# Kernel tuning notes

Hardware: AMD Instinct MI355X
Metric: run time of the kernel (lower is better)

## Reference

```python
import jax, jax.numpy as jnp
import numpy as np

N_HEADS = 16
K_CH = 1024 // N_HEADS  # 64
SCALE = 1.0 / np.sqrt(K_CH)


def setup_inputs() -> dict:
    key = jax.random.key(0)
    ks = jax.random.split(key, 10)
    B, C, T = 4, 1024, 2048
    Cout = 1024
    xavier = lambda k, o, i: jax.random.uniform(k, (o, i), jnp.float32, -1.0, 1.0) * np.sqrt(6.0 / (o + i))
    return {
        "x": jax.random.normal(ks[0], (B, C, T), jnp.float32),
        "c": jax.random.normal(ks[1], (B, C, T), jnp.float32),
        "Wq": xavier(ks[2], C, C), "bq": jnp.zeros((C,), jnp.float32),
        "Wk": xavier(ks[3], C, C), "bk": jnp.zeros((C,), jnp.float32),
        "Wv": xavier(ks[4], C, C), "bv": jnp.zeros((C,), jnp.float32),
        "Wo": xavier(ks[5], Cout, C), "bo": jnp.zeros((Cout,), jnp.float32),
    }


def reference(x, c, Wq, bq, Wk, bk, Wv, bv, Wo, bo):
    B, C, T = x.shape
    H, K = N_HEADS, K_CH
    # 1x1 Conv1d == per-timestep linear: [O,C] @ [B,C,T] -> [B,O,T]
    q = jnp.einsum('oc,bct->bot', Wq, x) + bq[None, :, None]
    k = jnp.einsum('oc,bct->bot', Wk, c) + bk[None, :, None]
    v = jnp.einsum('oc,bct->bot', Wv, c) + bv[None, :, None]
    # split heads: b (h k) t -> b h k t
    q = q.reshape(B, H, K, T)
    k = k.reshape(B, H, K, -1)
    v = v.reshape(B, H, K, -1)
    scores = jnp.einsum('bhkt,bhks->bhts', q, k) * SCALE  # [B,H,Tt,Ts]
    p = jax.nn.softmax(scores, axis=-1)
    out = jnp.einsum('bhts,bhks->bhkt', p, v)  # b h k t
    out = out.reshape(B, H * K, T)
    return jnp.einsum('oc,bct->bot', Wo, out) + bo[None, :, None]
```

## Files before the change

kernel.cpp:

```cpp
#include <hip/hip_runtime.h>
#include <stdint.h>

typedef __bf16 bf16x8 __attribute__((ext_vector_type(8)));
typedef float f32x4 __attribute__((ext_vector_type(4)));
typedef float f32x16 __attribute__((ext_vector_type(16)));
typedef unsigned u32x2 __attribute__((ext_vector_type(2)));
typedef unsigned u32x4 __attribute__((ext_vector_type(4)));

#define LOG2E 1.44269504088896340736f
#define ATT_SCALE 0.125f
#define CL (ATT_SCALE * LOG2E)
#define SWZ(row, colb) ((colb) ^ (((row) & 7) << 4))

#define GLOAD_LDS16(gp, lp)                                                  \
  __builtin_amdgcn_global_load_lds(                                          \
      (const __attribute__((address_space(1))) void*)(gp),                   \
      (__attribute__((address_space(3))) void*)(lp), 16, 0, 0)

__device__ __forceinline__ unsigned short f2bf(float f) {
  unsigned int x = __float_as_uint(f);
  x += 0x7fffu + ((x >> 16) & 1u);
  return (unsigned short)(x >> 16);
}

__device__ __forceinline__ float fexp2(float x) {
#if __has_builtin(__builtin_amdgcn_exp2f)
  return __builtin_amdgcn_exp2f(x);
#else
  return exp2f(x);
#endif
}

__device__ __forceinline__ unsigned cvtpk(float lo, float hi) {
  unsigned r;
  asm("v_cvt_pk_bf16_f32 %0, %1, %2" : "=v"(r) : "v"(lo), "v"(hi));
  return r;
}

__device__ __forceinline__ u32x2 plswap(unsigned a, unsigned b) {
  asm("v_permlane32_swap_b32 %0, %1" : "+v"(a), "+v"(b));
  u32x2 r;
  r[0] = a;
  r[1] = b;
  return r;
}

__global__ __launch_bounds__(256) void prep_inputs(
    const float* __restrict__ x, const float* __restrict__ c,
    const float* __restrict__ Wq, const float* __restrict__ Wk,
    const float* __restrict__ Wv, const float* __restrict__ Wo,
    unsigned short* __restrict__ xT, unsigned short* __restrict__ cT,
    unsigned short* __restrict__ wqb, unsigned short* __restrict__ wkb,
    unsigned short* __restrict__ wvb, unsigned short* __restrict__ wob) {
  const int C = 1024, T = 2048;
  int z = blockIdx.z;
  if (z >= 8) {
    int sel = z - 8;
    int bi = blockIdx.y * 64 + blockIdx.x;
    if (bi >= 512) return;
    const float* in = sel == 0 ? Wq : sel == 1 ? Wk : sel == 2 ? Wv : Wo;
    unsigned short* out = sel == 0 ? wqb : sel == 1 ? wkb : sel == 2 ? wvb : wob;
    float scale = sel == 0 ? CL : 1.0f;
    int off = (bi * 256 + threadIdx.x) * 8;
    #pragma unroll
    for (int p = 0; p < 2; ++p) {
      float4 v = *(const float4*)(in + off + p * 4);
      ushort4 o;
      o.x = f2bf(v.x * scale); o.y = f2bf(v.y * scale);
      o.z = f2bf(v.z * scale); o.w = f2bf(v.w * scale);
      *(ushort4*)(out + off + p * 4) = o;
    }
    return;
  }
  __shared__ unsigned short tile[32][33];
  const float* in = (z < 4) ? x : c;
  unsigned short* out = (z < 4) ? xT : cT;
  int b = z & 3;
  int t0 = blockIdx.x * 32, c0 = blockIdx.y * 32;
  int tx = threadIdx.x & 31, ty = threadIdx.x >> 5;
  const float* src = in + ((size_t)b * C + c0) * T + t0;
  #pragma unroll
  for (int i = 0; i < 4; ++i) {
    int cc = ty + i * 8;
    tile[cc][tx] = f2bf(src[(size_t)cc * T + tx]);
  }
  __syncthreads();
  unsigned short* dst = out + ((size_t)b * T + t0) * C + c0;
  #pragma unroll
  for (int i = 0; i < 4; ++i) {
    int tt = ty + i * 8;
    dst[(size_t)tt * C + tx] = tile[tx][tt];
  }
}

template <int NT, int OUT_F32>
__device__ __forceinline__ void gemm_core128(
    const unsigned short* __restrict__ A, const unsigned short* __restrict__ B,
    void* __restrict__ Cv, const float* __restrict__ bias, int bias_is_m,
    float bs, int m0, int n0, int ldC) {
  __shared__ __align__(16) char lds[3 * 16384];
  const int tid = threadIdx.x;
  const int l = tid & 63, w = tid >> 6;
  const int g = l >> 4, j = l & 15;
  const int wr = w >> 1, wc = w & 1;

  const int r0 = tid >> 3;
  const int slotp = (tid & 7) ^ (r0 & 7);
  const int mloc = r0 * 2 + (slotp >> 2);
  const int kg = slotp & 3;
  const unsigned short* ga0 = A + (size_t)(m0 + mloc) * 1024 + kg * 8;
  const unsigned short* ga1 = A + (size_t)(m0 + 64 + mloc) * 1024 + kg * 8;
  const unsigned short* gb0 = B + (size_t)(n0 + mloc) * 1024 + kg * 8;
  const unsigned short* gb1 = B + (size_t)(n0 + 64 + mloc) * 1024 + kg * 8;

  auto stage = [&](char* buf) {
    GLOAD_LDS16(ga0, buf + tid * 16);
    GLOAD_LDS16(ga1, buf + 4096 + tid * 16);
    GLOAD_LDS16(gb0, buf + 8192 + tid * 16);
    GLOAD_LDS16(gb1, buf + 12288 + tid * 16);
    ga0 += 32; ga1 += 32; gb0 += 32; gb1 += 32;
  };

  f32x4 acc[4][4] = {};

  stage(lds);
  stage(lds + 16384);

  char* bufc = lds;
  char* bufs = lds + 2 * 16384;

  for (int t = 0; t < NT; ++t) {
    if (t == NT - 1) asm volatile("s_waitcnt vmcnt(0)" ::: "memory");
    else             asm volatile("s_waitcnt vmcnt(4)" ::: "memory");
    __builtin_amdgcn_s_barrier();
    asm volatile("" ::: "memory");
    if (t < NT - 2) stage(bufs);

    bf16x8 af[4], bfr[4];
    #pragma unroll
    for (int mf = 0; mf < 4; ++mf) {
      int m = wr * 64 + mf * 16 + j;
      int rp = m >> 1;
      int cb = ((m & 1) * 64 + g * 16) ^ ((rp & 7) << 4);
      af[mf] = *(const bf16x8*)(bufc + rp * 128 + cb);
    }
    #pragma unroll
    for (int nf = 0; nf < 4; ++nf) {
      int n = wc * 64 + nf * 16 + j;
      int rp = n >> 1;
      int cb = ((n & 1) * 64 + g * 16) ^ ((rp & 7) << 4);
      bfr[nf] = *(const bf16x8*)(bufc + 8192 + rp * 128 + cb);
    }
    #pragma unroll
    for (int mf = 0; mf < 4; ++mf)
      #pragma unroll
      for (int nf = 0; nf < 4; ++nf)
        acc[mf][nf] = __builtin_amdgcn_mfma_f32_16x16x32_bf16(af[mf], bfr[nf], acc[mf][nf], 0, 0, 0);

    bufc += 16384; if (bufc == lds + 49152) bufc = lds;
    bufs += 16384; if (bufs == lds + 49152) bufs = lds;
  }

  #pragma unroll
  for (int mf = 0; mf < 4; ++mf) {
    #pragma unroll
    for (int rr = 0; rr < 4; ++rr) {
      int m = m0 + wr * 64 + mf * 16 + g * 4 + rr;
      float bm = bias_is_m ? bias[m] * bs : 0.f;
      #pragma unroll
      for (int nf = 0; nf < 4; ++nf) {
        int n = n0 + wc * 64 + nf * 16 + j;
        float val = acc[mf][nf][rr] + bm + (bias_is_m ? 0.f : bias[n] * bs);
        if (OUT_F32) ((float*)Cv)[(size_t)m * ldC + n] = val;
        else ((unsigned short*)Cv)[(size_t)m * ldC + n] = f2bf(val);
      }
    }
  }
}

__global__ __launch_bounds__(256, 3) void qkv_gemm3(
    const unsigned short* __restrict__ xT, const unsigned short* __restrict__ cT,
    const unsigned short* __restrict__ wq, const unsigned short* __restrict__ wk,
    const unsigned short* __restrict__ wv,
    const float* __restrict__ bq, const float* __restrict__ bk,
    const float* __restrict__ bv,
    unsigned short* __restrict__ QT, unsigned short* __restrict__ KT,
    unsigned short* __restrict__ Vb) {
  const size_t sBT = (size_t)2048 * 1024;
  const int id = (blockIdx.x & 7) * 192 + (blockIdx.x >> 3);
  const int op = id >> 9;
  const int r = id & 511;
  const int z = r >> 7;
  const unsigned short *A, *B;
  unsigned short* Cp;
  const float* bias;
  int m0, n0, ldC, bias_is_m;
  float bs;
  if (op == 2) {
    n0 = (r & 15) * 128; m0 = ((r >> 4) & 7) * 128;
    A = wv; B = cT + z * sBT; Cp = Vb + z * (size_t)1024 * 2048;
    bias = bv; ldC = 2048; bias_is_m = 1; bs = 1.0f;
  } else {
    n0 = (r & 7) * 128; m0 = ((r >> 3) & 15) * 128;
    A = (op == 0 ? xT : cT) + z * sBT;
    B = (op == 0 ? wq : wk);
    Cp = (op == 0 ? QT : KT) + z * sBT;
    bias = (op == 0 ? bq : bk); ldC = 1024; bias_is_m = 0;
    bs = (op == 0) ? CL : 1.0f;
  }
  gemm_core128<32, 0>(A, B, Cp, bias, bias_is_m, bs, m0, n0, ldC);
}

__global__ __launch_bounds__(256, 3) void gemm_out3(
    const unsigned short* __restrict__ Wo, const unsigned short* __restrict__ OT,
    float* __restrict__ Out, const float* __restrict__ bias) {
  const size_t sBT = (size_t)2048 * 1024;
  const int id = (blockIdx.x & 7) * 64 + (blockIdx.x >> 3);
  const int z = id >> 7;
  const int m0 = ((id >> 4) & 7) * 128, n0 = (id & 15) * 128;
  gemm_core128<32, 1>(Wo, OT + z * sBT, Out + z * (size_t)1024 * 2048,
                      bias, 1, 1.0f, m0, n0, 2048);
}

__global__ __launch_bounds__(256, 2) void attn_kernel8(const unsigned short* __restrict__ QT,
                                                       const unsigned short* __restrict__ KT,
                                                       const unsigned short* __restrict__ V,
                                                       unsigned short* __restrict__ OT) {
  __shared__ __align__(16) char kv[3][16384];
  __shared__ float lbuf[4][32];

  const int fid = blockIdx.x;
  const int xcd = fid & 7, idx = fid >> 3;
  const int bh = ((idx & 7) << 3) | xcd;
  const int tblk = idx >> 3;
  const int b = bh >> 4, h = bh & 15;

  const int tid = threadIdx.x;
  const int w = tid >> 6, l = tid & 63, lo5 = l & 31, hi = l >> 5;
  const int tq0 = tblk * 256 + w * 64;

  bf16x8 q[2][4];
  {
    const unsigned short* Qb = QT + ((size_t)(b * 2048 + tq0 + lo5)) * 1024 + h * 64 + hi * 8;
    #pragma unroll
    for (int tb = 0; tb < 2; ++tb)
      #pragma unroll
      for (int kb = 0; kb < 4; ++kb)
        q[tb][kb] = *(const bf16x8*)(Qb + (size_t)tb * 32 * 1024 + kb * 16);
  }

  f32x16 o[2][2] = {};
  float lr[2] = {0.f, 0.f};

  const int srow0 = tid >> 3, sslot = tid & 7;
  const int ch0 = sslot ^ (srow0 & 7);
  const int ch1 = sslot ^ ((32 + srow0) & 7);
  const unsigned short* kp0 = KT + ((size_t)(b * 2048 + srow0)) * 1024 + h * 64 + ch0 * 8;
  const unsigned short* kp1 = KT + ((size_t)(b * 2048 + 32 + srow0)) * 1024 + h * 64 + ch1 * 8;
  const unsigned short* vp0 = V + ((size_t)(b * 1024 + h * 64 + srow0)) * 2048 + ch0 * 8;
  const unsigned short* vp1 = V + ((size_t)(b * 1024 + h * 64 + 32 + srow0)) * 2048 + ch1 * 8;

  auto stage = [&](char* buf) {
    GLOAD_LDS16(kp0, buf + tid * 16);
    GLOAD_LDS16(kp1, buf + 4096 + tid * 16);
    GLOAD_LDS16(vp0, buf + 8192 + tid * 16);
    GLOAD_LDS16(vp1, buf + 12288 + tid * 16);
    kp0 += 64 * 1024; kp1 += 64 * 1024;
    vp0 += 64; vp1 += 64;
  };

  stage(kv[0]);
  stage(kv[1]);

  char* bufc = kv[0];
  char* bufs = kv[2];

  for (int t = 0; t < 32; ++t) {
    if (t == 31) asm volatile("s_waitcnt vmcnt(0)" ::: "memory");
    else         asm volatile("s_waitcnt vmcnt(4)" ::: "memory");
    __builtin_amdgcn_s_barrier();
    asm volatile("" ::: "memory");
    if (t < 30) stage(bufs);

    const char* Ks = bufc;
    const char* Vs = bufc + 8192;

    bf16x8 ka[2][4];
    #pragma unroll
    for (int sblk = 0; sblk < 2; ++sblk)
      #pragma unroll
      for (int kb = 0; kb < 4; ++kb) {
        int row = sblk * 32 + lo5;
        ka[sblk][kb] = *(const bf16x8*)(Ks + row * 128 + SWZ(row, kb * 32 + hi * 16));
      }

    u32x4 pa[2][4];
    #pragma unroll
    for (int tb = 0; tb < 2; ++tb) {
      f32x16 p0 = {}, p1 = {};
      #pragma unroll
      for (int kb = 0; kb < 4; ++kb) {
        p0 = __builtin_amdgcn_mfma_f32_32x32x16_bf16(ka[0][kb], q[tb][kb], p0, 0, 0, 0);
        p1 = __builtin_amdgcn_mfma_f32_32x32x16_bf16(ka[1][kb], q[tb][kb], p1, 0, 0, 0);
      }

      float ls0 = 0.f, ls1 = 0.f, ls2 = 0.f, ls3 = 0.f;
      #pragma unroll
      for (int r = 0; r < 16; r += 4) {
        float e0 = fexp2(p0[r]), e1 = fexp2(p0[r + 1]), e2 = fexp2(p0[r + 2]), e3 = fexp2(p0[r + 3]);
        p0[r] = e0; p0[r + 1] = e1; p0[r + 2] = e2; p0[r + 3] = e3;
        ls0 += e0; ls1 += e1; ls2 += e2; ls3 += e3;
      }
      #pragma unroll
      for (int r = 0; r < 16; r += 4) {
        float e0 = fexp2(p1[r]), e1 = fexp2(p1[r + 1]), e2 = fexp2(p1[r + 2]), e3 = fexp2(p1[r + 3]);
        p1[r] = e0; p1[r + 1] = e1; p1[r + 2] = e2; p1[r + 3] = e3;
        ls0 += e0; ls1 += e1; ls2 += e2; ls3 += e3;
      }
      lr[tb] += (ls0 + ls1) + (ls2 + ls3);

      u32x2 ra = plswap(cvtpk(p0[0], p0[1]), cvtpk(p0[4], p0[5]));
      u32x2 rb = plswap(cvtpk(p0[2], p0[3]), cvtpk(p0[6], p0[7]));
      pa[tb][0] = (u32x4){ra[0], rb[0], ra[1], rb[1]};
      u32x2 rc = plswap(cvtpk(p0[8], p0[9]), cvtpk(p0[12], p0[13]));
      u32x2 rd = plswap(cvtpk(p0[10], p0[11]), cvtpk(p0[14], p0[15]));
      pa[tb][1] = (u32x4){rc[0], rd[0], rc[1], rd[1]};
      u32x2 re = plswap(cvtpk(p1[0], p1[1]), cvtpk(p1[4], p1[5]));
      u32x2 rf = plswap(cvtpk(p1[2], p1[3]), cvtpk(p1[6], p1[7]));
      pa[tb][2] = (u32x4){re[0], rf[0], re[1], rf[1]};
      u32x2 rg = plswap(cvtpk(p1[8], p1[9]), cvtpk(p1[12], p1[13]));
      u32x2 rh = plswap(cvtpk(p1[10], p1[11]), cvtpk(p1[14], p1[15]));
      pa[tb][3] = (u32x4){rg[0], rh[0], rg[1], rh[1]};
    }

    #pragma unroll
    for (int sb = 0; sb < 4; ++sb)
      #pragma unroll
      for (int kb2 = 0; kb2 < 2; ++kb2) {
        int row = kb2 * 32 + lo5;
        bf16x8 vb = *(const bf16x8*)(Vs + row * 128 + SWZ(row, sb * 32 + hi * 16));
        o[0][kb2] = __builtin_amdgcn_mfma_f32_32x32x16_bf16(
            __builtin_bit_cast(bf16x8, pa[0][sb]), vb, o[0][kb2], 0, 0, 0);
        o[1][kb2] = __builtin_amdgcn_mfma_f32_32x32x16_bf16(
            __builtin_bit_cast(bf16x8, pa[1][sb]), vb, o[1][kb2], 0, 0, 0);
      }

    bufc += 16384; if (bufc == kv[0] + 49152) bufc = kv[0];
    bufs += 16384; if (bufs == kv[0] + 49152) bufs = kv[0];
  }

  #pragma unroll
  for (int tb = 0; tb < 2; ++tb) {
    float lt = lr[tb] + __shfl_xor(lr[tb], 32);
    if (hi == 0) lbuf[w][lo5] = 1.0f / lt;
    unsigned short* Ob = OT + ((size_t)(b * 2048 + tq0 + tb * 32)) * 1024 + h * 64 + lo5;
    #pragma unroll
    for (int r = 0; r < 16; ++r) {
      int srow = (r & 3) + 8 * (r >> 2) + 4 * hi;
      float inv = lbuf[w][srow];
      Ob[(size_t)srow * 1024 + 0]  = f2bf(o[tb][0][r] * inv);
      Ob[(size_t)srow * 1024 + 32] = f2bf(o[tb][1][r] * inv);
    }
  }
}

extern "C" void kernel_launch(void* const* d_in, const int* in_sizes, int n_in,
                              void* d_out, int out_size, void* d_ws, size_t ws_size,
                              hipStream_t stream) {
  const float* x  = (const float*)d_in[0];
  const float* c  = (const float*)d_in[1];
  const float* Wq = (const float*)d_in[2];
  const float* bq = (const float*)d_in[3];
  const float* Wk = (const float*)d_in[4];
  const float* bk = (const float*)d_in[5];
  const float* Wv = (const float*)d_in[6];
  const float* bv = (const float*)d_in[7];
  const float* Wo = (const float*)d_in[8];
  const float* bo = (const float*)d_in[9];

  const size_t MB = 1024 * 1024;
  char* ws = (char*)d_ws;
  unsigned short* wqb = (unsigned short*)(ws + 0 * MB);
  unsigned short* wkb = (unsigned short*)(ws + 2 * MB);
  unsigned short* wvb = (unsigned short*)(ws + 4 * MB);
  unsigned short* wob = (unsigned short*)(ws + 6 * MB);
  unsigned short* xT  = (unsigned short*)(ws + 8 * MB);
  unsigned short* cT  = (unsigned short*)(ws + 24 * MB);
  unsigned short* QT  = (unsigned short*)(ws + 40 * MB);
  unsigned short* KT  = (unsigned short*)(ws + 56 * MB);
  unsigned short* Vb  = (unsigned short*)(ws + 72 * MB);
  unsigned short* OT  = xT;

  prep_inputs<<<dim3(64, 32, 12), 256, 0, stream>>>(x, c, Wq, Wk, Wv, Wo,
                                                    xT, cT, wqb, wkb, wvb, wob);

  qkv_gemm3<<<dim3(1536), 256, 0, stream>>>(xT, cT, wqb, wkb, wvb, bq, bk, bv, QT, KT, Vb);

  attn_kernel8<<<dim3(512), 256, 0, stream>>>(QT, KT, Vb, OT);

  gemm_out3<<<dim3(512), 256, 0, stream>>>(wob, OT, (float*)d_out, bo);
}
```

Baseline: 181.7 us.

## Split QKV GEMM into specialized Q/K kernel with register-streamed weights

Replaces the fused QKV projection kernel with two launches. A new Q/K kernel stages only the activation tile in LDS through a triple-buffered async global-to-LDS pipeline and streams weight fragments straight into double-buffered registers. The V projection keeps the generic GEMM core in its own launch. The aim is to cut LDS traffic and barriers in the Q/K GEMM, at the cost of one extra launch, an occupancy hint lowered to 2, and weight loads from global memory that are not shared across waves.

Measured after the change: 203.2 us. 11.8% more time.

```diff
diff --git a/kernel.cpp b/kernel.cpp
--- a/kernel.cpp
+++ b/kernel.cpp
@@ -178,37 +178,124 @@
   }
 }
 
-__global__ __launch_bounds__(256, 3) void qkv_gemm3(
+__global__ __launch_bounds__(256, 2) void qkv_qk(
     const unsigned short* __restrict__ xT, const unsigned short* __restrict__ cT,
     const unsigned short* __restrict__ wq, const unsigned short* __restrict__ wk,
-    const unsigned short* __restrict__ wv,
     const float* __restrict__ bq, const float* __restrict__ bk,
-    const float* __restrict__ bv,
-    unsigned short* __restrict__ QT, unsigned short* __restrict__ KT,
-    unsigned short* __restrict__ Vb) {
+    unsigned short* __restrict__ QT, unsigned short* __restrict__ KT) {
+  __shared__ __align__(16) char lds[3 * 8192];
   const size_t sBT = (size_t)2048 * 1024;
-  const int id = (blockIdx.x & 7) * 192 + (blockIdx.x >> 3);
+
+  const int id = (blockIdx.x & 7) * 128 + (blockIdx.x >> 3);
   const int op = id >> 9;
   const int r = id & 511;
   const int z = r >> 7;
-  const unsigned short *A, *B;
-  unsigned short* Cp;
-  const float* bias;
-  int m0, n0, ldC, bias_is_m;
-  float bs;
-  if (op == 2) {
-    n0 = (r & 15) * 128; m0 = ((r >> 4) & 7) * 128;
-    A = wv; B = cT + z * sBT; Cp = Vb + z * (size_t)1024 * 2048;
-    bias = bv; ldC = 2048; bias_is_m = 1; bs = 1.0f;
-  } else {
-    n0 = (r & 7) * 128; m0 = ((r >> 3) & 15) * 128;
-    A = (op == 0 ? xT : cT) + z * sBT;
-    B = (op == 0 ? wq : wk);
-    Cp = (op == 0 ? QT : KT) + z * sBT;
-    bias = (op == 0 ? bq : bk); ldC = 1024; bias_is_m = 0;
-    bs = (op == 0) ? CL : 1.0f;
-  }
-  gemm_core128<32, 0>(A, B, Cp, bias, bias_is_m, bs, m0, n0, ldC);
+  const int m0 = ((r >> 3) & 15) * 128, n0 = (r & 7) * 128;
+  const unsigned short* A = (op == 0 ? xT : cT) + z * sBT;
+  const unsigned short* Bw = (op == 0 ? wq : wk);
+  unsigned short* Cp = (op == 0 ? QT : KT) + z * sBT;
+  const float* bias = (op == 0 ? bq : bk);
+  const float bs = (op == 0) ? CL : 1.0f;
+
+  const int tid = threadIdx.x;
+  const int l = tid & 63, w = tid >> 6;
+  const int g = l >> 4, j = l & 15;
+  const int wr = w >> 1, wc = w & 1;
+
+  const int r0 = tid >> 3;
+  const int slotp = (tid & 7) ^ (r0 & 7);
+  const int mloc = r0 * 2 + (slotp >> 2);
+  const int kg = slotp & 3;
+  const unsigned short* ga0 = A + (size_t)(m0 + mloc) * 1024 + kg * 8;
+  const unsigned short* ga1 = A + (size_t)(m0 + 64 + mloc) * 1024 + kg * 8;
+
+  const unsigned short* pb = Bw + (size_t)(n0 + wc * 64 + j) * 1024 + g * 8;
+
+  f32x4 acc[4][4] = {};
+  bf16x8 bfrA[4], bfrB[4];
+
+  GLOAD_LDS16(ga0, lds + tid * 16);
+  GLOAD_LDS16(ga1, lds + 4096 + tid * 16);
+  ga0 += 32; ga1 += 32;
+  GLOAD_LDS16(ga0, lds + 8192 + tid * 16);
+  GLOAD_LDS16(ga1, lds + 12288 + tid * 16);
+  ga0 += 32; ga1 += 32;
+  bfrA[0] = *(const bf16x8*)(pb);
+  bfrA[1] = *(const bf16x8*)(pb + 16 * 1024);
+  bfrA[2] = *(const bf16x8*)(pb + 32 * 1024);
+  bfrA[3] = *(const bf16x8*)(pb + 48 * 1024);
+  pb += 32;
+
+  char* bufc = lds;
+  char* bufs = lds + 2 * 8192;
+
+#define QK_BODY(USEB, LOADB, DO_LOADB, DO_STAGE, WAITN)                      \
+  do {                                                                       \
+    asm volatile("s_waitcnt vmcnt(" #WAITN ")" ::: "memory");                \
+    __builtin_amdgcn_s_barrier();                                            \
+    asm volatile("" ::: "memory");                                           \
+    if (DO_LOADB) {                                                          \
+      LOADB[0] = *(const bf16x8*)(pb);                                       \
+      LOADB[1] = *(const bf16x8*)(pb + 16 * 1024);                           \
+      LOADB[2] = *(const bf16x8*)(pb + 32 * 1024);                           \
+      LOADB[3] = *(const bf16x8*)(pb + 48 * 1024);                           \
+      pb += 32;                                                              \
+    }                                                                        \
+    if (DO_STAGE) {                                                          \
+      GLOAD_LDS16(ga0, bufs + tid * 16);                                     \
+      GLOAD_LDS16(ga1, bufs + 4096 + tid * 16);                              \
+      ga0 += 32; ga1 += 32;                                                  \
+    }                                                                        \
+    bf16x8 af[4];                                                            \
+    _Pragma("unroll")                                                        \
+    for (int mf = 0; mf < 4; ++mf) {                                         \
+      int m = wr * 64 + mf * 16 + j;                                         \
+      int rp = m >> 1;                                                       \
+      int cb = ((m & 1) * 64 + g * 16) ^ ((rp & 7) << 4);                    \
+      af[mf] = *(const bf16x8*)(bufc + rp * 128 + cb);                       \
+    }                                                                        \
+    _Pragma("unroll")                                                        \
+    for (int mf = 0; mf < 4; ++mf)                                           \
+      _Pragma("unroll")                                                      \
+      for (int nf = 0; nf < 4; ++nf)                                         \
+        acc[mf][nf] = __builtin_amdgcn_mfma_f32_16x16x32_bf16(               \
+            af[mf], USEB[nf], acc[mf][nf], 0, 0, 0);                         \
+    bufc += 8192; if (bufc == lds + 24576) bufc = lds;                       \
+    bufs += 8192; if (bufs == lds + 24576) bufs = lds;                       \
+  } while (0)
+
+  for (int t = 0; t < 30; t += 2) {
+    QK_BODY(bfrA, bfrB, 1, 1, 6);
+    QK_BODY(bfrB, bfrA, 1, 1, 6);
+  }
+  QK_BODY(bfrA, bfrB, 1, 0, 6);
+  QK_BODY(bfrB, bfrA, 0, 0, 4);
+#undef QK_BODY
+
+  #pragma unroll
+  for (int mf = 0; mf < 4; ++mf) {
+    #pragma unroll
+    for (int rr = 0; rr < 4; ++rr) {
+      int m = m0 + wr * 64 + mf * 16 + g * 4 + rr;
+      #pragma unroll
+      for (int nf = 0; nf < 4; ++nf) {
+        int n = n0 + wc * 64 + nf * 16 + j;
+        Cp[(size_t)m * 1024 + n] = f2bf(acc[mf][nf][rr] + bias[n] * bs);
+      }
+    }
+  }
+}
+
+__global__ __launch_bounds__(256, 3) void qkv_v(
+    const unsigned short* __restrict__ cT, const unsigned short* __restrict__ wv,
+    const float* __restrict__ bv, unsigned short* __restrict__ Vb) {
+  const size_t sBT = (size_t)2048 * 1024;
+  const int id = (blockIdx.x & 7) * 64 + (blockIdx.x >> 3);
+  const int z = id >> 7;
+  const int r = id & 127;
+  const int n0 = (r & 15) * 128, m0 = ((r >> 4) & 7) * 128;
+  gemm_core128<32, 0>(wv, cT + z * sBT, Vb + z * (size_t)1024 * 2048,
+                      bv, 1, 1.0f, m0, n0, 2048);
 }
 
 __global__ __launch_bounds__(256, 3) void gemm_out3(
@@ -394,7 +481,8 @@
   prep_inputs<<<dim3(64, 32, 12), 256, 0, stream>>>(x, c, Wq, Wk, Wv, Wo,
                                                     xT, cT, wqb, wkb, wvb, wob);
 
-  qkv_gemm3<<<dim3(1536), 256, 0, stream>>>(xT, cT, wqb, wkb, wvb, bq, bk, bv, QT, KT, Vb);
+  qkv_qk<<<dim3(1024), 256, 0, stream>>>(xT, cT, wqb, wkb, bq, bk, QT, KT);
+  qkv_v<<<dim3(512), 256, 0, stream>>>(cT, wvb, bv, Vb);
 
   attn_kernel8<<<dim3(512), 256, 0, stream>>>(QT, KT, Vb, OT);
 
```

## Use 256x128 tiles with triple-buffered LDS pipeline in QKV GEMM

Applied to the files above, without the earlier changes.

The QKV projection GEMM moves from the shared 128x128 core to a dedicated 256x128 tile kernel. Each warp now computes 128x64 outputs with 8x4 MFMA fragments, and K tiles are staged through a three-slot LDS ring filled by global_load_lds, with explicit vmcnt waits. Larger tiles raise arithmetic intensity and cut the block count in half. The cost is more registers and LDS (72KB), so occupancy drops to 2 blocks per CU.

Result: slower. 192.9 us (+6.2%).

```diff
diff --git a/kernel.cpp b/kernel.cpp
--- a/kernel.cpp
+++ b/kernel.cpp
@@ -178,7 +178,7 @@
   }
 }
 
-__global__ __launch_bounds__(256, 3) void qkv_gemm3(
+__global__ __launch_bounds__(256, 2) void qkv_gemm4(
     const unsigned short* __restrict__ xT, const unsigned short* __restrict__ cT,
     const unsigned short* __restrict__ wq, const unsigned short* __restrict__ wk,
     const unsigned short* __restrict__ wv,
@@ -186,29 +186,118 @@
     const float* __restrict__ bv,
     unsigned short* __restrict__ QT, unsigned short* __restrict__ KT,
     unsigned short* __restrict__ Vb) {
+  __shared__ __align__(16) char lds[3 * 24576];
   const size_t sBT = (size_t)2048 * 1024;
-  const int id = (blockIdx.x & 7) * 192 + (blockIdx.x >> 3);
-  const int op = id >> 9;
-  const int r = id & 511;
-  const int z = r >> 7;
+
+  const int id = (blockIdx.x & 7) * 96 + (blockIdx.x >> 3);
+  const int op = id >> 8;
+  const int r = id & 255;
+  const int z = r >> 6;
+  const int r6 = r & 63;
+
   const unsigned short *A, *B;
   unsigned short* Cp;
   const float* bias;
   int m0, n0, ldC, bias_is_m;
   float bs;
   if (op == 2) {
-    n0 = (r & 15) * 128; m0 = ((r >> 4) & 7) * 128;
+    m0 = (r6 & 3) * 256; n0 = (r6 >> 2) * 128;
     A = wv; B = cT + z * sBT; Cp = Vb + z * (size_t)1024 * 2048;
     bias = bv; ldC = 2048; bias_is_m = 1; bs = 1.0f;
   } else {
-    n0 = (r & 7) * 128; m0 = ((r >> 3) & 15) * 128;
+    m0 = (r6 >> 3) * 256; n0 = (r6 & 7) * 128;
     A = (op == 0 ? xT : cT) + z * sBT;
     B = (op == 0 ? wq : wk);
     Cp = (op == 0 ? QT : KT) + z * sBT;
     bias = (op == 0 ? bq : bk); ldC = 1024; bias_is_m = 0;
     bs = (op == 0) ? CL : 1.0f;
   }
-  gemm_core128<32, 0>(A, B, Cp, bias, bias_is_m, bs, m0, n0, ldC);
+
+  const int tid = threadIdx.x;
+  const int l = tid & 63, w = tid >> 6;
+  const int g = l >> 4, j = l & 15;
+  const int wr = w >> 1, wc = w & 1;
+
+  const int r0 = tid >> 3;
+  const int slotp = (tid & 7) ^ (r0 & 7);
+  const int mloc = r0 * 2 + (slotp >> 2);
+  const int kg = slotp & 3;
+  const unsigned short* ga[4];
+  const unsigned short* gb[2];
+  #pragma unroll
+  for (int c2 = 0; c2 < 4; ++c2)
+    ga[c2] = A + (size_t)(m0 + c2 * 64 + mloc) * 1024 + kg * 8;
+  #pragma unroll
+  for (int c2 = 0; c2 < 2; ++c2)
+    gb[c2] = B + (size_t)(n0 + c2 * 64 + mloc) * 1024 + kg * 8;
+
+  auto stage = [&](char* buf) {
+    #pragma unroll
+    for (int c2 = 0; c2 < 4; ++c2) {
+      GLOAD_LDS16(ga[c2], buf + c2 * 4096 + tid * 16);
+      ga[c2] += 32;
+    }
+    #pragma unroll
+    for (int c2 = 0; c2 < 2; ++c2) {
+      GLOAD_LDS16(gb[c2], buf + 16384 + c2 * 4096 + tid * 16);
+      gb[c2] += 32;
+    }
+  };
+
+  f32x4 acc[8][4] = {};
+
+  stage(lds);
+  stage(lds + 24576);
+
+  char* bufc = lds;
+  char* bufs = lds + 2 * 24576;
+
+  for (int t = 0; t < 32; ++t) {
+    if (t == 31) asm volatile("s_waitcnt vmcnt(0)" ::: "memory");
+    else         asm volatile("s_waitcnt vmcnt(6)" ::: "memory");
+    __builtin_amdgcn_s_barrier();
+    asm volatile("" ::: "memory");
+    if (t < 30) stage(bufs);
+
+    bf16x8 af[8], bfr[4];
+    #pragma unroll
+    for (int mf = 0; mf < 8; ++mf) {
+      int m = wr * 128 + mf * 16 + j;
+      int rp = m >> 1;
+      int cb = ((m & 1) * 64 + g * 16) ^ ((rp & 7) << 4);
+      af[mf] = *(const bf16x8*)(bufc + rp * 128 + cb);
+    }
+    #pragma unroll
+    for (int nf = 0; nf < 4; ++nf) {
+      int n = wc * 64 + nf * 16 + j;
+      int rp = n >> 1;
+      int cb = ((n & 1) * 64 + g * 16) ^ ((rp & 7) << 4);
+      bfr[nf] = *(const bf16x8*)(bufc + 16384 + rp * 128 + cb);
+    }
+    #pragma unroll
+    for (int mf = 0; mf < 8; ++mf)
+      #pragma unroll
+      for (int nf = 0; nf < 4; ++nf)
+        acc[mf][nf] = __builtin_amdgcn_mfma_f32_16x16x32_bf16(af[mf], bfr[nf], acc[mf][nf], 0, 0, 0);
+
+    bufc += 24576; if (bufc == lds + 73728) bufc = lds;
+    bufs += 24576; if (bufs == lds + 73728) bufs = lds;
+  }
+
+  #pragma unroll
+  for (int mf = 0; mf < 8; ++mf) {
+    #pragma unroll
+    for (int rr = 0; rr < 4; ++rr) {
+      int m = m0 + wr * 128 + mf * 16 + g * 4 + rr;
+      float bm = bias_is_m ? bias[m] * bs : 0.f;
+      #pragma unroll
+      for (int nf = 0; nf < 4; ++nf) {
+        int n = n0 + wc * 64 + nf * 16 + j;
+        float val = acc[mf][nf][rr] + bm + (bias_is_m ? 0.f : bias[n] * bs);
+        Cp[(size_t)m * ldC + n] = f2bf(val);
+      }
+    }
+  }
 }
 
 __global__ __launch_bounds__(256, 3) void gemm_out3(
@@ -394,7 +483,7 @@
   prep_inputs<<<dim3(64, 32, 12), 256, 0, stream>>>(x, c, Wq, Wk, Wv, Wo,
                                                     xT, cT, wqb, wkb, wvb, wob);
 
-  qkv_gemm3<<<dim3(1536), 256, 0, stream>>>(xT, cT, wqb, wkb, wvb, bq, bk, bv, QT, KT, Vb);
+  qkv_gemm4<<<dim3(768), 256, 0, stream>>>(xT, cT, wqb, wkb, wvb, bq, bk, bv, QT, KT, Vb);
 
   attn_kernel8<<<dim3(512), 256, 0, stream>>>(QT, KT, Vb, OT);
 
```
